# Performance work log

Hardware: AMD Instinct MI355X
Metric: run time of the kernel (lower is better)

The kernel has to match this reference:

```python
import jax, jax.numpy as jnp
from jax import lax
import numpy as np

RADIUS = 0.2
NSAMPLE = 32


def setup_inputs() -> dict:
    key = jax.random.key(0)
    ks = jax.random.split(key, 6)
    B, N, C = 4, 16384, 64
    xyz = jax.random.uniform(ks[0], (B, N, 3), dtype=jnp.float32)
    points = jax.random.normal(ks[1], (B, N, C), dtype=jnp.float32)
    w1 = jax.random.normal(ks[2], (64, C + 3), dtype=jnp.float32) * 0.05
    b1 = jnp.zeros((64,), jnp.float32)
    w2 = jax.random.normal(ks[3], (128, 64), dtype=jnp.float32) * 0.05
    b2 = jnp.zeros((128,), jnp.float32)
    return {"xyz": xyz, "points": points, "w1": w1, "b1": b1, "w2": w2, "b2": b2, "npoint": 1024}


def farthest_point_sampling(xyz, npoint):
    # xyz: (B,N,3). Deterministic start at index 0 (original uses a random start).
    B, N, _ = xyz.shape
    bidx = jnp.arange(B)

    def step(carry, _):
        distance, farthest = carry
        centroid = xyz[bidx, farthest]  # (B,3)
        dist = jnp.sum((xyz - centroid[:, None, :]) ** 2, axis=-1)  # (B,N)
        distance = jnp.minimum(distance, dist)
        nxt = jnp.argmax(distance, axis=-1)
        return (distance, nxt), farthest

    init = (jnp.full((B, N), 1e10, xyz.dtype), jnp.zeros((B,), jnp.int32))
    _, cents = lax.scan(step, init, None, length=npoint)  # (npoint,B)
    return cents.T  # (B,npoint)


def ball_query(xyz, new_xyz, radius, nsample):
    # xyz:(B,N,3) new_xyz:(B,S,3) -> (B,S,nsample) int indices
    N = xyz.shape[1]
    sqrdists = jnp.sum((new_xyz[:, :, None, :] - xyz[:, None, :, :]) ** 2, axis=-1)  # (B,S,N)
    idx = jnp.where(sqrdists > radius ** 2, N, jnp.arange(N))
    idx = jnp.sort(idx, axis=-1)[:, :, :nsample]
    first = idx[:, :, :1]
    return jnp.where(idx == N, first, idx)


def index_points(points, idx):
    # points:(B,N,C) idx:(B,...) -> (B,...,C)
    return jax.vmap(lambda p, i: p[i])(points, idx)


def reference(xyz, points, w1, b1, w2, b2, npoint):
    centroids = farthest_point_sampling(xyz, npoint)  # (B,S)
    new_xyz = index_points(xyz, centroids)  # (B,S,3)
    group_idx = ball_query(xyz, new_xyz, RADIUS, NSAMPLE)  # (B,S,K)
    grouped_xyz = index_points(xyz, group_idx)  # (B,S,K,3)
    grouped_xyz_norm = grouped_xyz - new_xyz[:, :, None, :]
    grouped_points = index_points(points, group_idx)  # (B,S,K,C)
    feats = jnp.concatenate([grouped_xyz_norm, grouped_points], axis=-1)  # (B,S,K,C+3)
    h = jax.nn.relu(jnp.einsum('bskc,oc->bsko', feats, w1) + b1)
    h = jax.nn.relu(jnp.einsum('bskc,oc->bsko', h, w2) + b2)  # (B,S,K,out)
    new_points = jnp.max(h, axis=2)  # (B,S,out)
    return (new_xyz, new_points)
```

## Files before the change

### kernel.cpp

```cpp
#include <hip/hip_runtime.h>

#define BB 4
#define NN 16384
#define CC 64
#define NPOINT 1024
#define NSAMPLE 32

#define FPS_T 1024
#define NCHUNK 256
#define NCELL 4096

#define REPEAT16(M) M(0) M(1) M(2) M(3) M(4) M(5) M(6) M(7) \
                    M(8) M(9) M(10) M(11) M(12) M(13) M(14) M(15)

__global__ __launch_bounds__(FPS_T) void fps_kernel(const float* __restrict__ xyz,
                                                    float* __restrict__ new_xyz,
                                                    float4* __restrict__ sorted) {
    #pragma clang fp contract(off)
    extern __shared__ char smem_raw[];
    float2* sxy  = (float2*)smem_raw;
    int*    hist = (int*)(smem_raw + 131072);
    float*  outc = (float*)(smem_raw + 131072);
    float*  lox  = (float*)(smem_raw + 147456);
    float*  loy  = lox + 272;
    float*  loz  = loy + 272;
    float*  hix  = loz + 272;
    float*  hiy  = hix + 272;
    float*  hiz  = hiy + 272;
    float4* wbc  = (float4*)(smem_raw + 153984);
    unsigned long long* slot = (unsigned long long*)(smem_raw + 154496);
    int*    wsum = (int*)(smem_raw + 154528);

    const int b    = blockIdx.x;
    const int tid  = threadIdx.x;
    const int lane = tid & 63;
    const int wv   = tid >> 6;
    const float* bx = xyz + (size_t)b * NN * 3;
    float4* sb = sorted + (size_t)b * NN;

    #pragma unroll
    for (int j = 0; j < 4; ++j) hist[j * FPS_T + tid] = 0;
    __syncthreads();

    #pragma unroll
    for (int j = 0; j < 16; ++j) {
        const int p = j * FPS_T + tid;
        const float x = bx[p * 3 + 0], y = bx[p * 3 + 1], z = bx[p * 3 + 2];
        int cx = (int)(x * 16.0f); cx = cx > 15 ? 15 : (cx < 0 ? 0 : cx);
        int cy = (int)(y * 16.0f); cy = cy > 15 ? 15 : (cy < 0 ? 0 : cy);
        int cz = (int)(z * 16.0f); cz = cz > 15 ? 15 : (cz < 0 ? 0 : cz);
        int code = 0;
        #pragma unroll
        for (int i = 0; i < 4; ++i)
            code |= (((cx >> i) & 1) << (3 * i)) |
                    (((cy >> i) & 1) << (3 * i + 1)) |
                    (((cz >> i) & 1) << (3 * i + 2));
        atomicAdd(&hist[code], 1);
    }
    __syncthreads();

    {
        const int h0 = hist[4 * tid + 0], h1 = hist[4 * tid + 1];
        const int h2 = hist[4 * tid + 2], h3 = hist[4 * tid + 3];
        const int s  = h0 + h1 + h2 + h3;
        int v = s;
        #pragma unroll
        for (int o = 1; o < 64; o <<= 1) {
            const int u = __shfl_up(v, o, 64);
            if (lane >= o) v += u;
        }
        if (lane == 63) wsum[wv] = v;
        __syncthreads();
        int base = 0;
        for (int w = 0; w < wv; ++w) base += wsum[w];
        const int e0 = base + v - s;
        hist[4 * tid + 0] = e0;
        hist[4 * tid + 1] = e0 + h0;
        hist[4 * tid + 2] = e0 + h0 + h1;
        hist[4 * tid + 3] = e0 + h0 + h1 + h2;
    }
    __syncthreads();

    #pragma unroll
    for (int j = 0; j < 16; ++j) {
        const int p = j * FPS_T + tid;
        const float x = bx[p * 3 + 0], y = bx[p * 3 + 1], z = bx[p * 3 + 2];
        int cx = (int)(x * 16.0f); cx = cx > 15 ? 15 : (cx < 0 ? 0 : cx);
        int cy = (int)(y * 16.0f); cy = cy > 15 ? 15 : (cy < 0 ? 0 : cy);
        int cz = (int)(z * 16.0f); cz = cz > 15 ? 15 : (cz < 0 ? 0 : cz);
        int code = 0;
        #pragma unroll
        for (int i = 0; i < 4; ++i)
            code |= (((cx >> i) & 1) << (3 * i)) |
                    (((cy >> i) & 1) << (3 * i + 1)) |
                    (((cz >> i) & 1) << (3 * i + 2));
        const int slotg = atomicAdd(&hist[code], 1);
        sb[slotg]  = make_float4(x, y, z, __int_as_float(p));
        sxy[slotg] = make_float2(x, y);
    }
    __syncthreads();

#define DECLZ(k) float z##k; unsigned long long key##k;
    REPEAT16(DECLZ)
#undef DECLZ
    float abx0 = 0.f, aby0 = 0.f, abz0 = 0.f, abx1 = 0.f, aby1 = 0.f, abz1 = 0.f;

#define AABBPRE(k) { const int g = wv + ((k) << 4);                       \
    const float4 pt = sb[(g << 6) + lane];                                \
    z##k = pt.z;                                                          \
    key##k = (((unsigned long long)__float_as_uint(1e10f)) << 32) |       \
             ((unsigned long long)(0x3FFFu -                              \
                    (unsigned)__float_as_int(pt.w)) << 4);                \
    float mnx = pt.x, mxx = pt.x, mny = pt.y, mxy = pt.y,                 \
          mnz = pt.z, mxz = pt.z;                                         \
    _Pragma("unroll")                                                     \
    for (int m = 32; m >= 1; m >>= 1) {                                   \
        mnx = fminf(mnx, __shfl_xor(mnx, m, 64));                         \
        mxx = fmaxf(mxx, __shfl_xor(mxx, m, 64));                         \
        mny = fminf(mny, __shfl_xor(mny, m, 64));                         \
        mxy = fmaxf(mxy, __shfl_xor(mxy, m, 64));                         \
        mnz = fminf(mnz, __shfl_xor(mnz, m, 64));                         \
        mxz = fmaxf(mxz, __shfl_xor(mxz, m, 64));                         \
    }                                                                     \
    if (lane == (k)) { abx0 = mnx; abx1 = mxx; aby0 = mny; aby1 = mxy;    \
                       abz0 = mnz; abz1 = mxz; } }
    REPEAT16(AABBPRE)
#undef AABBPRE
    if (tid == 0) { slot[0] = 0ull; slot[1] = 0ull; slot[2] = 0ull; slot[3] = 0ull; }
    __syncthreads();

    unsigned long long bkey = 0ull;
    int bestk = 0;
    int holder_ln = 0;
    float hx = 0.f, hy = 0.f, hz = 0.f;
    float cub = 1e10f;

    float ccx = bx[0], ccy = bx[1], ccz = bx[2];
    float prev_wd = 1e10f;

    for (int it = 0; it < NPOINT; ++it) {
        asm volatile("" : "+v"(z0), "+v"(z1), "+v"(z2),  "+v"(z3),
                          "+v"(z4), "+v"(z5), "+v"(z6),  "+v"(z7),
                          "+v"(z8), "+v"(z9), "+v"(z10), "+v"(z11),
                          "+v"(z12), "+v"(z13), "+v"(z14), "+v"(z15));

        if (tid == 0) {
            outc[it * 3 + 0] = ccx;
            outc[it * 3 + 1] = ccy;
            outc[it * 3 + 2] = ccz;
        }

        bool active = false;
        if (lane < 16) {
            const float dxl = fmaxf(fmaxf(abx0 - ccx, ccx - abx1), 0.0f);
            const float dyl = fmaxf(fmaxf(aby0 - ccy, ccy - aby1), 0.0f);
            const float dzl = fmaxf(fmaxf(abz0 - ccz, ccz - abz1), 0.0f);
            const float mind2 = dxl * dxl + dyl * dyl + dzl * dzl;
            const float bound = fminf(prev_wd, cub);
            active = !(mind2 > bound * 1.001f);
            if (active) {
                const float dxm = fmaxf(ccx - abx0, abx1 - ccx);
                const float dym = fmaxf(ccy - aby0, aby1 - ccy);
                const float dzm = fmaxf(ccz - abz0, abz1 - ccz);
                const float maxd2 = dxm * dxm + dym * dym + dzm * dzm;
                cub = fminf(cub, maxd2);
            }
        }
        const unsigned amask = (unsigned)(__ballot(active) & 0xFFFFull);

        bool lredo = false;
#define UPD(k) if (amask & (1u << (k))) {                                 \
            const int g = wv + ((k) << 4);                                \
            const float2 xy = sxy[(g << 6) + lane];                       \
            const float dx = xy.x - ccx;                                  \
            const float dy = xy.y - ccy;                                  \
            const float dz = z##k - ccz;                                  \
            const float t  = (dx * dx + dy * dy) + dz * dz;               \
            const float dold = __uint_as_float((unsigned)(key##k >> 32)); \
            if (t < dold) {                                               \
                key##k = (((unsigned long long)__float_as_uint(t)) << 32) \
                         | (key##k & 0xFFFFFFFFull);                      \
                lredo |= ((k) == bestk);                                  \
            }                                                             \
        }
        if (amask & 0x000Fu) { UPD(0)  UPD(1)  UPD(2)  UPD(3)  }
        if (amask & 0x00F0u) { UPD(4)  UPD(5)  UPD(6)  UPD(7)  }
        if (amask & 0x0F00u) { UPD(8)  UPD(9)  UPD(10) UPD(11) }
        if (amask & 0xF000u) { UPD(12) UPD(13) UPD(14) UPD(15) }
#undef UPD

        if (lredo) {
            bkey = 0ull; bestk = 0;
#define LM(k) if (key##k > bkey) { bkey = key##k; bestk = (k); }
            REPEAT16(LM)
#undef LM
        }

        const unsigned long long rb = __ballot(lredo);
        if ((rb >> holder_ln) & 1ull) {
            unsigned long long m = bkey;
            #pragma unroll
            for (int s = 32; s >= 1; s >>= 1) {
                const unsigned long long o = __shfl_xor(m, s, 64);
                m = o > m ? o : m;
            }
            holder_ln = __ffsll((long long)__ballot(bkey == m)) - 1;
            if (lane == holder_ln) {
                const float2 xy = sxy[((wv + (bestk << 4)) << 6) + lane];
                float zz = z0;
#define ZS(k) zz = (bestk == (k)) ? z##k : zz;
                REPEAT16(ZS)
#undef ZS
                hx = xy.x; hy = xy.y; hz = zz;
            }
        }

        if (lane == holder_ln) {
            wbc[(it & 1) * 16 + wv] = make_float4(hx, hy, hz, 0.0f);
            atomicMax(&slot[it & 3], bkey | (unsigned long long)wv);
        }
        if (tid == 0) slot[(it + 1) & 3] = 0ull;
        __syncthreads();

        const unsigned long long wk = slot[it & 3];
        prev_wd = __uint_as_float((unsigned)(wk >> 32));
        const int wwv = (int)(wk & 0xFull);
        const float4 wf = wbc[(it & 1) * 16 + wwv];
        ccx = wf.x; ccy = wf.y; ccz = wf.z;
    }

    __syncthreads();
    float* outb = new_xyz + (size_t)b * NPOINT * 3;
    #pragma unroll
    for (int j = 0; j < 3; ++j) {
        const int idx = j * FPS_T + tid;
        outb[idx] = outc[idx];
    }
}

__global__ __launch_bounds__(256) void ballq_kernel(const float* __restrict__ xyz,
                                                    const float* __restrict__ new_xyz,
                                                    int* __restrict__ gidx) {
    #pragma clang fp contract(off)
    const int lane = threadIdx.x & 63;
    const int q    = blockIdx.x * 4 + (threadIdx.x >> 6);
    const int b    = q >> 10;
    const float* bx = xyz + (size_t)b * NN * 3;
    const float* nx = new_xyz + (size_t)q * 3;
    const float cx = nx[0], cy = nx[1], cz = nx[2];
    const float rad2 = 0.04f;

    int* out  = gidx + (size_t)q * NSAMPLE;
    int taken = 0;
    int first = NN - 1;

    for (int chunk = 0; chunk < NN / 64 && taken < NSAMPLE; ++chunk) {
        const int   i  = chunk * 64 + lane;
        const float dx = cx - bx[i * 3 + 0];
        const float dy = cy - bx[i * 3 + 1];
        const float dz = cz - bx[i * 3 + 2];
        const float t  = dx * dx + dy * dy + dz * dz;
        const bool ok  = !(t > rad2);
        const unsigned long long m = __ballot(ok);
        const int cnt = __popcll(m);
        if (taken == 0 && cnt > 0) first = chunk * 64 + (__ffsll((long long)m) - 1);
        if (ok) {
            const int rank = taken + __popcll(m & ((1ull << lane) - 1ull));
            if (rank < NSAMPLE) out[rank] = i;
        }
        taken += cnt;
    }
    const int sat = taken < NSAMPLE ? taken : NSAMPLE;
    if (lane >= sat && lane < NSAMPLE) out[lane] = (taken > 0) ? first : (NN - 1);
}

__global__ __launch_bounds__(256) void mlp_kernel(const float* __restrict__ xyz,
                                                  const float* __restrict__ points,
                                                  const float* __restrict__ w1,
                                                  const float* __restrict__ b1,
                                                  const float* __restrict__ w2,
                                                  const float* __restrict__ b2,
                                                  const float* __restrict__ new_xyz,
                                                  const int*   __restrict__ gidx,
                                                  float* __restrict__ new_points) {
    __shared__ __align__(16) float feats[32][68];
    __shared__ __align__(16) float h1s[32][64];
    __shared__ float pmax[2][128];

    const int q = blockIdx.x;
    const int b = q >> 10;
    const int t = threadIdx.x;

    {
        const int k  = t >> 3;
        const int l8 = t & 7;
        const int gi = gidx[q * 32 + k];
        const float* prow = points + ((size_t)b * NN + gi) * CC;
        const float4 v0 = *(const float4*)(prow + l8 * 8);
        const float4 v1 = *(const float4*)(prow + l8 * 8 + 4);
        *(float4*)&feats[k][4 + l8 * 8] = v0;
        *(float4*)&feats[k][8 + l8 * 8] = v1;
        if (l8 == 0) {
            const float* pr = xyz + ((size_t)b * NN + gi) * 3;
            const float* nr = new_xyz + (size_t)q * 3;
            feats[k][0] = pr[0] - nr[0];
            feats[k][1] = pr[1] - nr[1];
            feats[k][2] = pr[2] - nr[2];
        }
    }

    const int c1 = t & 63;
    float w1r[67];
    #pragma unroll
    for (int j = 0; j < 67; ++j) w1r[j] = w1[c1 * 67 + j];
    const float bb1 = b1[c1];
    __syncthreads();

    const int kg = t >> 6;
    #pragma unroll
    for (int kk = 0; kk < 8; ++kk) {
        const int kr = kg * 8 + kk;
        float acc = bb1;
        acc += feats[kr][0] * w1r[0] + feats[kr][1] * w1r[1] + feats[kr][2] * w1r[2];
        #pragma unroll
        for (int j = 0; j < 64; j += 4) {
            const float4 f = *(const float4*)&feats[kr][4 + j];
            acc += f.x * w1r[3 + j] + f.y * w1r[4 + j] + f.z * w1r[5 + j] + f.w * w1r[6 + j];
        }
        h1s[kr][c1] = fmaxf(acc, 0.0f);
    }

    const int o2 = t & 127;
    const int kh = t >> 7;
    float w2r[64];
    #pragma unroll
    for (int j = 0; j < 64; ++j) w2r[j] = w2[o2 * 64 + j];
    const float bb2 = b2[o2];
    __syncthreads();

    float mx = -INFINITY;
    #pragma unroll
    for (int kk = 0; kk < 16; ++kk) {
        const int kr = kh * 16 + kk;
        float acc = bb2;
        #pragma unroll
        for (int j = 0; j < 64; j += 4) {
            const float4 h = *(const float4*)&h1s[kr][j];
            acc += h.x * w2r[j] + h.y * w2r[j + 1] + h.z * w2r[j + 2] + h.w * w2r[j + 3];
        }
        mx = fmaxf(mx, fmaxf(acc, 0.0f));
    }
    pmax[kh][o2] = mx;
    __syncthreads();
    if (t < 128) {
        new_points[(size_t)q * 128 + t] = fmaxf(pmax[0][t], pmax[1][t]);
    }
}

extern "C" void kernel_launch(void* const* d_in, const int* in_sizes, int n_in,
                              void* d_out, int out_size, void* d_ws, size_t ws_size,
                              hipStream_t stream) {
    const float* xyz    = (const float*)d_in[0];
    const float* points = (const float*)d_in[1];
    const float* w1     = (const float*)d_in[2];
    const float* b1     = (const float*)d_in[3];
    const float* w2     = (const float*)d_in[4];
    const float* b2     = (const float*)d_in[5];

    float* out_newxyz    = (float*)d_out;
    float* out_newpoints = (float*)d_out + (size_t)BB * NPOINT * 3;
    int*    gidx    = (int*)d_ws;
    float4* sortbuf = (float4*)((char*)d_ws + (size_t)512 * 1024);

    const int fps_lds = 154816;
    (void)hipFuncSetAttribute((const void*)fps_kernel,
                              hipFuncAttributeMaxDynamicSharedMemorySize,
                              fps_lds);

    fps_kernel<<<BB, FPS_T, fps_lds, stream>>>(xyz, out_newxyz, sortbuf);
    ballq_kernel<<<(BB * NPOINT) / 4, 256, 0, stream>>>(xyz, out_newxyz, gidx);
    mlp_kernel<<<BB * NPOINT, 256, 0, stream>>>(xyz, points, w1, b1, w2, b2,
                                                out_newxyz, gidx, out_newpoints);
}
```

Baseline: 1.590 ms.

## Halve FPS block to 8 waves with 32 chunks per lane and split argmax slots

The farthest-point-sampling kernel now runs with 512 threads (8 waves), so each lane holds 32 point chunks in registers instead of 16, with AABB culling extended to 32 chunks. The per-iteration cross-wave argmax uses four separate atomic slots, reduced after the barrier, and the winning centroid is broadcast by shuffling a speculatively loaded per-wave candidate. The aim is cheaper per-iteration barriers and less atomic contention in the serial 1024-step loop. In exchange each wave does twice the per-lane work and needs many more registers, which could cause spills.

```diff
diff --git a/kernel.cpp b/kernel.cpp
--- a/kernel.cpp
+++ b/kernel.cpp
@@ -6,30 +6,27 @@
 #define NPOINT 1024
 #define NSAMPLE 32
 
-#define FPS_T 1024
+#define FPS_T 512
+#define NWAVE 8
 #define NCHUNK 256
 #define NCELL 4096
 
-#define REPEAT16(M) M(0) M(1) M(2) M(3) M(4) M(5) M(6) M(7) \
-                    M(8) M(9) M(10) M(11) M(12) M(13) M(14) M(15)
-
-__global__ __launch_bounds__(FPS_T) void fps_kernel(const float* __restrict__ xyz,
-                                                    float* __restrict__ new_xyz,
-                                                    float4* __restrict__ sorted) {
+#define REPEAT32(M) M(0) M(1) M(2) M(3) M(4) M(5) M(6) M(7) \
+                    M(8) M(9) M(10) M(11) M(12) M(13) M(14) M(15) \
+                    M(16) M(17) M(18) M(19) M(20) M(21) M(22) M(23) \
+                    M(24) M(25) M(26) M(27) M(28) M(29) M(30) M(31)
+
+__global__ __launch_bounds__(FPS_T, 2) void fps_kernel(const float* __restrict__ xyz,
+                                                       float* __restrict__ new_xyz,
+                                                       float4* __restrict__ sorted) {
     #pragma clang fp contract(off)
     extern __shared__ char smem_raw[];
     float2* sxy  = (float2*)smem_raw;
     int*    hist = (int*)(smem_raw + 131072);
     float*  outc = (float*)(smem_raw + 131072);
-    float*  lox  = (float*)(smem_raw + 147456);
-    float*  loy  = lox + 272;
-    float*  loz  = loy + 272;
-    float*  hix  = loz + 272;
-    float*  hiy  = hix + 272;
-    float*  hiz  = hiy + 272;
-    float4* wbc  = (float4*)(smem_raw + 153984);
-    unsigned long long* slot = (unsigned long long*)(smem_raw + 154496);
-    int*    wsum = (int*)(smem_raw + 154528);
+    float4* wbc  = (float4*)(smem_raw + 147456);
+    unsigned long long* slot4 = (unsigned long long*)(smem_raw + 147712);
+    int*    wsum = (int*)(smem_raw + 147840);
 
     const int b    = blockIdx.x;
     const int tid  = threadIdx.x;
@@ -39,11 +36,11 @@
     float4* sb = sorted + (size_t)b * NN;
 
     #pragma unroll
-    for (int j = 0; j < 4; ++j) hist[j * FPS_T + tid] = 0;
-    __syncthreads();
-
-    #pragma unroll
-    for (int j = 0; j < 16; ++j) {
+    for (int j = 0; j < 8; ++j) hist[j * FPS_T + tid] = 0;
+    __syncthreads();
+
+    #pragma unroll
+    for (int j = 0; j < 32; ++j) {
         const int p = j * FPS_T + tid;
         const float x = bx[p * 3 + 0], y = bx[p * 3 + 1], z = bx[p * 3 + 2];
         int cx = (int)(x * 16.0f); cx = cx > 15 ? 15 : (cx < 0 ? 0 : cx);
@@ -60,9 +57,10 @@
     __syncthreads();
 
     {
-        const int h0 = hist[4 * tid + 0], h1 = hist[4 * tid + 1];
-        const int h2 = hist[4 * tid + 2], h3 = hist[4 * tid + 3];
-        const int s  = h0 + h1 + h2 + h3;
+        const int b8 = 8 * tid;
+        const int h0 = hist[b8+0], h1 = hist[b8+1], h2 = hist[b8+2], h3 = hist[b8+3];
+        const int h4 = hist[b8+4], h5 = hist[b8+5], h6 = hist[b8+6], h7 = hist[b8+7];
+        const int s  = h0 + h1 + h2 + h3 + h4 + h5 + h6 + h7;
         int v = s;
         #pragma unroll
         for (int o = 1; o < 64; o <<= 1) {
@@ -73,16 +71,20 @@
         __syncthreads();
         int base = 0;
         for (int w = 0; w < wv; ++w) base += wsum[w];
-        const int e0 = base + v - s;
-        hist[4 * tid + 0] = e0;
-        hist[4 * tid + 1] = e0 + h0;
-        hist[4 * tid + 2] = e0 + h0 + h1;
-        hist[4 * tid + 3] = e0 + h0 + h1 + h2;
-    }
-    __syncthreads();
-
-    #pragma unroll
-    for (int j = 0; j < 16; ++j) {
+        int e = base + v - s;
+        hist[b8+0] = e; e += h0;
+        hist[b8+1] = e; e += h1;
+        hist[b8+2] = e; e += h2;
+        hist[b8+3] = e; e += h3;
+        hist[b8+4] = e; e += h4;
+        hist[b8+5] = e; e += h5;
+        hist[b8+6] = e; e += h6;
+        hist[b8+7] = e;
+    }
+    __syncthreads();
+
+    #pragma unroll
+    for (int j = 0; j < 32; ++j) {
         const int p = j * FPS_T + tid;
         const float x = bx[p * 3 + 0], y = bx[p * 3 + 1], z = bx[p * 3 + 2];
         int cx = (int)(x * 16.0f); cx = cx > 15 ? 15 : (cx < 0 ? 0 : cx);
@@ -101,11 +103,11 @@
     __syncthreads();
 
 #define DECLZ(k) float z##k; unsigned long long key##k;
-    REPEAT16(DECLZ)
+    REPEAT32(DECLZ)
 #undef DECLZ
     float abx0 = 0.f, aby0 = 0.f, abz0 = 0.f, abx1 = 0.f, aby1 = 0.f, abz1 = 0.f;
 
-#define AABBPRE(k) { const int g = wv + ((k) << 4);                       \
+#define AABBPRE(k) { const int g = wv + ((k) << 3);                       \
     const float4 pt = sb[(g << 6) + lane];                                \
     z##k = pt.z;                                                          \
     key##k = (((unsigned long long)__float_as_uint(1e10f)) << 32) |       \
@@ -124,10 +126,19 @@
     }                                                                     \
     if (lane == (k)) { abx0 = mnx; abx1 = mxx; aby0 = mny; aby1 = mxy;    \
                        abz0 = mnz; abz1 = mxz; } }
-    REPEAT16(AABBPRE)
+    REPEAT32(AABBPRE)
 #undef AABBPRE
-    if (tid == 0) { slot[0] = 0ull; slot[1] = 0ull; slot[2] = 0ull; slot[3] = 0ull; }
-    __syncthreads();
+    if (tid < 16) slot4[tid] = 0ull;
+    __syncthreads();
+
+    asm volatile("" : "+v"(z0), "+v"(z1), "+v"(z2),  "+v"(z3),
+                      "+v"(z4), "+v"(z5), "+v"(z6),  "+v"(z7),
+                      "+v"(z8), "+v"(z9), "+v"(z10), "+v"(z11),
+                      "+v"(z12), "+v"(z13), "+v"(z14), "+v"(z15));
+    asm volatile("" : "+v"(z16), "+v"(z17), "+v"(z18), "+v"(z19),
+                      "+v"(z20), "+v"(z21), "+v"(z22), "+v"(z23),
+                      "+v"(z24), "+v"(z25), "+v"(z26), "+v"(z27),
+                      "+v"(z28), "+v"(z29), "+v"(z30), "+v"(z31));
 
     unsigned long long bkey = 0ull;
     int bestk = 0;
@@ -139,11 +150,6 @@
     float prev_wd = 1e10f;
 
     for (int it = 0; it < NPOINT; ++it) {
-        asm volatile("" : "+v"(z0), "+v"(z1), "+v"(z2),  "+v"(z3),
-                          "+v"(z4), "+v"(z5), "+v"(z6),  "+v"(z7),
-                          "+v"(z8), "+v"(z9), "+v"(z10), "+v"(z11),
-                          "+v"(z12), "+v"(z13), "+v"(z14), "+v"(z15));
-
         if (tid == 0) {
             outc[it * 3 + 0] = ccx;
             outc[it * 3 + 1] = ccy;
@@ -151,7 +157,7 @@
         }
 
         bool active = false;
-        if (lane < 16) {
+        if (lane < 32) {
             const float dxl = fmaxf(fmaxf(abx0 - ccx, ccx - abx1), 0.0f);
             const float dyl = fmaxf(fmaxf(aby0 - ccy, ccy - aby1), 0.0f);
             const float dzl = fmaxf(fmaxf(abz0 - ccz, ccz - abz1), 0.0f);
@@ -166,11 +172,11 @@
                 cub = fminf(cub, maxd2);
             }
         }
-        const unsigned amask = (unsigned)(__ballot(active) & 0xFFFFull);
+        const unsigned amask = (unsigned)(__ballot(active) & 0xFFFFFFFFull);
 
         bool lredo = false;
 #define UPD(k) if (amask & (1u << (k))) {                                 \
-            const int g = wv + ((k) << 4);                                \
+            const int g = wv + ((k) << 3);                                \
             const float2 xy = sxy[(g << 6) + lane];                       \
             const float dx = xy.x - ccx;                                  \
             const float dy = xy.y - ccy;                                  \
@@ -183,16 +189,20 @@
                 lredo |= ((k) == bestk);                                  \
             }                                                             \
         }
-        if (amask & 0x000Fu) { UPD(0)  UPD(1)  UPD(2)  UPD(3)  }
-        if (amask & 0x00F0u) { UPD(4)  UPD(5)  UPD(6)  UPD(7)  }
-        if (amask & 0x0F00u) { UPD(8)  UPD(9)  UPD(10) UPD(11) }
-        if (amask & 0xF000u) { UPD(12) UPD(13) UPD(14) UPD(15) }
+        if (amask & 0x0000000Fu) { UPD(0)  UPD(1)  UPD(2)  UPD(3)  }
+        if (amask & 0x000000F0u) { UPD(4)  UPD(5)  UPD(6)  UPD(7)  }
+        if (amask & 0x00000F00u) { UPD(8)  UPD(9)  UPD(10) UPD(11) }
+        if (amask & 0x0000F000u) { UPD(12) UPD(13) UPD(14) UPD(15) }
+        if (amask & 0x000F0000u) { UPD(16) UPD(17) UPD(18) UPD(19) }
+        if (amask & 0x00F00000u) { UPD(20) UPD(21) UPD(22) UPD(23) }
+        if (amask & 0x0F000000u) { UPD(24) UPD(25) UPD(26) UPD(27) }
+        if (amask & 0xF0000000u) { UPD(28) UPD(29) UPD(30) UPD(31) }
 #undef UPD
 
         if (lredo) {
             bkey = 0ull; bestk = 0;
 #define LM(k) if (key##k > bkey) { bkey = key##k; bestk = (k); }
-            REPEAT16(LM)
+            REPEAT32(LM)
 #undef LM
         }
 
@@ -206,33 +216,43 @@
             }
             holder_ln = __ffsll((long long)__ballot(bkey == m)) - 1;
             if (lane == holder_ln) {
-                const float2 xy = sxy[((wv + (bestk << 4)) << 6) + lane];
+                const float2 xy = sxy[((wv + (bestk << 3)) << 6) + lane];
                 float zz = z0;
 #define ZS(k) zz = (bestk == (k)) ? z##k : zz;
-                REPEAT16(ZS)
+                REPEAT32(ZS)
 #undef ZS
                 hx = xy.x; hy = xy.y; hz = zz;
             }
         }
 
         if (lane == holder_ln) {
-            wbc[(it & 1) * 16 + wv] = make_float4(hx, hy, hz, 0.0f);
-            atomicMax(&slot[it & 3], bkey | (unsigned long long)wv);
-        }
-        if (tid == 0) slot[(it + 1) & 3] = 0ull;
+            wbc[(it & 1) * 8 + wv] = make_float4(hx, hy, hz, 0.0f);
+            atomicMax(&slot4[(it & 3) * 4 + (wv & 3)],
+                      bkey | (unsigned long long)wv);
+        }
+        if (tid < 4) slot4[((it + 1) & 3) * 4 + tid] = 0ull;
         __syncthreads();
 
-        const unsigned long long wk = slot[it & 3];
+        const float4 spec = wbc[(it & 1) * 8 + (lane & 7)];
+        const unsigned long long s0 = slot4[(it & 3) * 4 + 0];
+        const unsigned long long s1 = slot4[(it & 3) * 4 + 1];
+        const unsigned long long s2 = slot4[(it & 3) * 4 + 2];
+        const unsigned long long s3 = slot4[(it & 3) * 4 + 3];
+        unsigned long long wk = s0;
+        if (s1 > wk) wk = s1;
+        if (s2 > wk) wk = s2;
+        if (s3 > wk) wk = s3;
         prev_wd = __uint_as_float((unsigned)(wk >> 32));
-        const int wwv = (int)(wk & 0xFull);
-        const float4 wf = wbc[(it & 1) * 16 + wwv];
-        ccx = wf.x; ccy = wf.y; ccz = wf.z;
+        const int wwv = (int)(wk & 0x7ull);
+        ccx = __shfl(spec.x, wwv, 64);
+        ccy = __shfl(spec.y, wwv, 64);
+        ccz = __shfl(spec.z, wwv, 64);
     }
 
     __syncthreads();
     float* outb = new_xyz + (size_t)b * NPOINT * 3;
     #pragma unroll
-    for (int j = 0; j < 3; ++j) {
+    for (int j = 0; j < 6; ++j) {
         const int idx = j * FPS_T + tid;
         outb[idx] = outc[idx];
     }
@@ -372,7 +392,7 @@
     int*    gidx    = (int*)d_ws;
     float4* sortbuf = (float4*)((char*)d_ws + (size_t)512 * 1024);
 
-    const int fps_lds = 154816;
+    const int fps_lds = 147904;
     (void)hipFuncSetAttribute((const void*)fps_kernel,
                               hipFuncAttributeMaxDynamicSharedMemorySize,
                               fps_lds);
```

Measured after the change: 2.181 ms. +37.1%, slower.

## Fuse FPS, ball query and MLP into one persistent kernel with progress flags

Applied to the files above, without the earlier changes.

Merges the three launches into one cooperative persistent kernel. Four blocks run farthest point sampling and publish each centroid plus a per-batch progress counter. The other 196 blocks poll that counter and run ball query and the MLP on groups of 8 centroids as soon as they exist, so the consumer work overlaps the serial FPS loop. Ball query now does a per-warp linear scan with early exit instead of the separate kernel. This risks spin-wait overhead, lower occupancy from 1024-thread blocks with large LDS, and deadlock if the blocks are not all co-resident in the fallback launch.

```diff
diff --git a/kernel.cpp b/kernel.cpp
--- a/kernel.cpp
+++ b/kernel.cpp
@@ -9,351 +9,359 @@
 #define FPS_T 1024
 #define NCHUNK 256
 #define NCELL 4096
+#define GRID_TOTAL 200
 
 #define REPEAT16(M) M(0) M(1) M(2) M(3) M(4) M(5) M(6) M(7) \
                     M(8) M(9) M(10) M(11) M(12) M(13) M(14) M(15)
 
-__global__ __launch_bounds__(FPS_T) void fps_kernel(const float* __restrict__ xyz,
-                                                    float* __restrict__ new_xyz,
-                                                    float4* __restrict__ sorted) {
-    #pragma clang fp contract(off)
+__global__ __launch_bounds__(FPS_T, 4) void fused_kernel(
+        const float* __restrict__ xyz, const float* __restrict__ points,
+        const float* __restrict__ w1,  const float* __restrict__ b1,
+        const float* __restrict__ w2,  const float* __restrict__ b2,
+        float* __restrict__ new_xyz,   float* __restrict__ new_points,
+        float4* __restrict__ sorted,   unsigned* __restrict__ prog) {
     extern __shared__ char smem_raw[];
-    float2* sxy  = (float2*)smem_raw;
-    int*    hist = (int*)(smem_raw + 131072);
-    float*  outc = (float*)(smem_raw + 131072);
-    float*  lox  = (float*)(smem_raw + 147456);
-    float*  loy  = lox + 272;
-    float*  loz  = loy + 272;
-    float*  hix  = loz + 272;
-    float*  hiy  = hix + 272;
-    float*  hiz  = hiy + 272;
-    float4* wbc  = (float4*)(smem_raw + 153984);
-    unsigned long long* slot = (unsigned long long*)(smem_raw + 154496);
-    int*    wsum = (int*)(smem_raw + 154528);
-
-    const int b    = blockIdx.x;
+
+    if (blockIdx.x < 4) {
+        #pragma clang fp contract(off)
+        float2* sxy  = (float2*)smem_raw;
+        int*    hist = (int*)(smem_raw + 131072);
+        float4* wbc  = (float4*)(smem_raw + 147456);
+        unsigned long long* slot = (unsigned long long*)(smem_raw + 147968);
+        int*    wsum = (int*)(smem_raw + 148000);
+
+        const int b    = blockIdx.x;
+        const int tid  = threadIdx.x;
+        const int lane = tid & 63;
+        const int wv   = tid >> 6;
+        const float* bx = xyz + (size_t)b * NN * 3;
+        float4* sb = sorted + (size_t)b * NN;
+        float* outg = new_xyz + (size_t)b * NPOINT * 3;
+
+        #pragma unroll
+        for (int j = 0; j < 4; ++j) hist[j * FPS_T + tid] = 0;
+        __syncthreads();
+
+        #pragma unroll
+        for (int j = 0; j < 16; ++j) {
+            const int p = j * FPS_T + tid;
+            const float x = bx[p * 3 + 0], y = bx[p * 3 + 1], z = bx[p * 3 + 2];
+            int cx = (int)(x * 16.0f); cx = cx > 15 ? 15 : (cx < 0 ? 0 : cx);
+            int cy = (int)(y * 16.0f); cy = cy > 15 ? 15 : (cy < 0 ? 0 : cy);
+            int cz = (int)(z * 16.0f); cz = cz > 15 ? 15 : (cz < 0 ? 0 : cz);
+            int code = 0;
+            #pragma unroll
+            for (int i = 0; i < 4; ++i)
+                code |= (((cx >> i) & 1) << (3 * i)) |
+                        (((cy >> i) & 1) << (3 * i + 1)) |
+                        (((cz >> i) & 1) << (3 * i + 2));
+            atomicAdd(&hist[code], 1);
+        }
+        __syncthreads();
+
+        {
+            const int h0 = hist[4 * tid + 0], h1 = hist[4 * tid + 1];
+            const int h2 = hist[4 * tid + 2], h3 = hist[4 * tid + 3];
+            const int s  = h0 + h1 + h2 + h3;
+            int v = s;
+            #pragma unroll
+            for (int o = 1; o < 64; o <<= 1) {
+                const int u = __shfl_up(v, o, 64);
+                if (lane >= o) v += u;
+            }
+            if (lane == 63) wsum[wv] = v;
+            __syncthreads();
+            int base = 0;
+            for (int w = 0; w < wv; ++w) base += wsum[w];
+            const int e0 = base + v - s;
+            hist[4 * tid + 0] = e0;
+            hist[4 * tid + 1] = e0 + h0;
+            hist[4 * tid + 2] = e0 + h0 + h1;
+            hist[4 * tid + 3] = e0 + h0 + h1 + h2;
+        }
+        __syncthreads();
+
+        #pragma unroll
+        for (int j = 0; j < 16; ++j) {
+            const int p = j * FPS_T + tid;
+            const float x = bx[p * 3 + 0], y = bx[p * 3 + 1], z = bx[p * 3 + 2];
+            int cx = (int)(x * 16.0f); cx = cx > 15 ? 15 : (cx < 0 ? 0 : cx);
+            int cy = (int)(y * 16.0f); cy = cy > 15 ? 15 : (cy < 0 ? 0 : cy);
+            int cz = (int)(z * 16.0f); cz = cz > 15 ? 15 : (cz < 0 ? 0 : cz);
+            int code = 0;
+            #pragma unroll
+            for (int i = 0; i < 4; ++i)
+                code |= (((cx >> i) & 1) << (3 * i)) |
+                        (((cy >> i) & 1) << (3 * i + 1)) |
+                        (((cz >> i) & 1) << (3 * i + 2));
+            const int slotg = atomicAdd(&hist[code], 1);
+            sb[slotg]  = make_float4(x, y, z, __int_as_float(p));
+            sxy[slotg] = make_float2(x, y);
+        }
+        __syncthreads();
+
+#define DECLZ(k) float z##k; unsigned long long key##k;
+        REPEAT16(DECLZ)
+#undef DECLZ
+        float abx0 = 0.f, aby0 = 0.f, abz0 = 0.f, abx1 = 0.f, aby1 = 0.f, abz1 = 0.f;
+
+#define AABBPRE(k) { const int g = wv + ((k) << 4);                       \
+        const float4 pt = sb[(g << 6) + lane];                            \
+        z##k = pt.z;                                                      \
+        key##k = (((unsigned long long)__float_as_uint(1e10f)) << 32) |   \
+                 ((unsigned long long)(0x3FFFu -                          \
+                        (unsigned)__float_as_int(pt.w)) << 4);            \
+        float mnx = pt.x, mxx = pt.x, mny = pt.y, mxy = pt.y,             \
+              mnz = pt.z, mxz = pt.z;                                     \
+        _Pragma("unroll")                                                 \
+        for (int m = 32; m >= 1; m >>= 1) {                               \
+            mnx = fminf(mnx, __shfl_xor(mnx, m, 64));                     \
+            mxx = fmaxf(mxx, __shfl_xor(mxx, m, 64));                     \
+            mny = fminf(mny, __shfl_xor(mny, m, 64));                     \
+            mxy = fmaxf(mxy, __shfl_xor(mxy, m, 64));                     \
+            mnz = fminf(mnz, __shfl_xor(mnz, m, 64));                     \
+            mxz = fmaxf(mxz, __shfl_xor(mxz, m, 64));                     \
+        }                                                                 \
+        if (lane == (k)) { abx0 = mnx; abx1 = mxx; aby0 = mny;            \
+                           aby1 = mxy; abz0 = mnz; abz1 = mxz; } }
+        REPEAT16(AABBPRE)
+#undef AABBPRE
+        if (tid < 4) slot[tid] = 0ull;
+        __syncthreads();
+
+        unsigned long long bkey = 0ull;
+        int bestk = 0;
+        int holder_ln = 0;
+        float hx = 0.f, hy = 0.f, hz = 0.f;
+        float cub = 1e10f;
+
+        float ccx = bx[0], ccy = bx[1], ccz = bx[2];
+        float prev_wd = 1e10f;
+
+        for (int it = 0; it < NPOINT; ++it) {
+            asm volatile("" : "+v"(z0), "+v"(z1), "+v"(z2),  "+v"(z3),
+                              "+v"(z4), "+v"(z5), "+v"(z6),  "+v"(z7),
+                              "+v"(z8), "+v"(z9), "+v"(z10), "+v"(z11),
+                              "+v"(z12), "+v"(z13), "+v"(z14), "+v"(z15));
+
+            if (wv == (it & 15) && lane == 0) {
+                unsigned* og = (unsigned*)(outg + it * 3);
+                __hip_atomic_store(og + 0, __float_as_uint(ccx),
+                                   __ATOMIC_RELAXED, __HIP_MEMORY_SCOPE_AGENT);
+                __hip_atomic_store(og + 1, __float_as_uint(ccy),
+                                   __ATOMIC_RELAXED, __HIP_MEMORY_SCOPE_AGENT);
+                __hip_atomic_store(og + 2, __float_as_uint(ccz),
+                                   __ATOMIC_RELAXED, __HIP_MEMORY_SCOPE_AGENT);
+                __hip_atomic_store(&prog[b], (unsigned)(it + 1),
+                                   __ATOMIC_RELEASE, __HIP_MEMORY_SCOPE_AGENT);
+            }
+
+            bool active = false;
+            if (lane < 16) {
+                const float dxl = fmaxf(fmaxf(abx0 - ccx, ccx - abx1), 0.0f);
+                const float dyl = fmaxf(fmaxf(aby0 - ccy, ccy - aby1), 0.0f);
+                const float dzl = fmaxf(fmaxf(abz0 - ccz, ccz - abz1), 0.0f);
+                const float mind2 = dxl * dxl + dyl * dyl + dzl * dzl;
+                const float bound = fminf(prev_wd, cub);
+                active = !(mind2 > bound * 1.001f);
+                if (active) {
+                    const float dxm = fmaxf(ccx - abx0, abx1 - ccx);
+                    const float dym = fmaxf(ccy - aby0, aby1 - ccy);
+                    const float dzm = fmaxf(ccz - abz0, abz1 - ccz);
+                    const float maxd2 = dxm * dxm + dym * dym + dzm * dzm;
+                    cub = fminf(cub, maxd2);
+                }
+            }
+            const unsigned amask = (unsigned)(__ballot(active) & 0xFFFFull);
+
+            bool lredo = false;
+#define UPD(k) if (amask & (1u << (k))) {                                 \
+                const int g = wv + ((k) << 4);                            \
+                const float2 xy = sxy[(g << 6) + lane];                   \
+                const float dx = xy.x - ccx;                              \
+                const float dy = xy.y - ccy;                              \
+                const float dz = z##k - ccz;                              \
+                const float t  = (dx * dx + dy * dy) + dz * dz;           \
+                const float dold = __uint_as_float((unsigned)(key##k >> 32)); \
+                if (t < dold) {                                           \
+                    key##k = (((unsigned long long)__float_as_uint(t)) << 32) \
+                             | (key##k & 0xFFFFFFFFull);                  \
+                    lredo |= ((k) == bestk);                              \
+                }                                                         \
+            }
+            if (amask & 0x000Fu) { UPD(0)  UPD(1)  UPD(2)  UPD(3)  }
+            if (amask & 0x00F0u) { UPD(4)  UPD(5)  UPD(6)  UPD(7)  }
+            if (amask & 0x0F00u) { UPD(8)  UPD(9)  UPD(10) UPD(11) }
+            if (amask & 0xF000u) { UPD(12) UPD(13) UPD(14) UPD(15) }
+#undef UPD
+
+            if (lredo) {
+                bkey = 0ull; bestk = 0;
+#define LM(k) if (key##k > bkey) { bkey = key##k; bestk = (k); }
+                REPEAT16(LM)
+#undef LM
+            }
+
+            const unsigned long long rb = __ballot(lredo);
+            if ((rb >> holder_ln) & 1ull) {
+                unsigned long long m = bkey;
+                #pragma unroll
+                for (int s = 32; s >= 1; s >>= 1) {
+                    const unsigned long long o = __shfl_xor(m, s, 64);
+                    m = o > m ? o : m;
+                }
+                holder_ln = __ffsll((long long)__ballot(bkey == m)) - 1;
+                if (lane == holder_ln) {
+                    const float2 xy = sxy[((wv + (bestk << 4)) << 6) + lane];
+                    float zz = z0;
+#define ZS(k) zz = (bestk == (k)) ? z##k : zz;
+                    REPEAT16(ZS)
+#undef ZS
+                    hx = xy.x; hy = xy.y; hz = zz;
+                }
+            }
+
+            if (lane == holder_ln) {
+                wbc[(it & 1) * 16 + wv] = make_float4(hx, hy, hz, 0.0f);
+                atomicMax(&slot[it & 3], bkey | (unsigned long long)wv);
+            }
+            if (tid == 0) slot[(it + 1) & 3] = 0ull;
+            __syncthreads();
+
+            const unsigned long long wk = slot[it & 3];
+            prev_wd = __uint_as_float((unsigned)(wk >> 32));
+            const int wwv = (int)(wk & 0xFull);
+            const float4 wf = wbc[(it & 1) * 16 + wwv];
+            ccx = wf.x; ccy = wf.y; ccz = wf.z;
+        }
+        return;
+    }
+
+    float* feats = (float*)smem_raw;
+    float* h1s   = (float*)(smem_raw + 69632);
+    int*   sgidx = (int*)(smem_raw + 135168);
+
+    const int ci   = blockIdx.x - 4;
+    const int NC   = (int)gridDim.x - 4;
     const int tid  = threadIdx.x;
     const int lane = tid & 63;
-    const int wv   = tid >> 6;
-    const float* bx = xyz + (size_t)b * NN * 3;
-    float4* sb = sorted + (size_t)b * NN;
-
-    #pragma unroll
-    for (int j = 0; j < 4; ++j) hist[j * FPS_T + tid] = 0;
-    __syncthreads();
-
-    #pragma unroll
-    for (int j = 0; j < 16; ++j) {
-        const int p = j * FPS_T + tid;
-        const float x = bx[p * 3 + 0], y = bx[p * 3 + 1], z = bx[p * 3 + 2];
-        int cx = (int)(x * 16.0f); cx = cx > 15 ? 15 : (cx < 0 ? 0 : cx);
-        int cy = (int)(y * 16.0f); cy = cy > 15 ? 15 : (cy < 0 ? 0 : cy);
-        int cz = (int)(z * 16.0f); cz = cz > 15 ? 15 : (cz < 0 ? 0 : cz);
-        int code = 0;
-        #pragma unroll
-        for (int i = 0; i < 4; ++i)
-            code |= (((cx >> i) & 1) << (3 * i)) |
-                    (((cy >> i) & 1) << (3 * i + 1)) |
-                    (((cz >> i) & 1) << (3 * i + 2));
-        atomicAdd(&hist[code], 1);
-    }
-    __syncthreads();
-
-    {
-        const int h0 = hist[4 * tid + 0], h1 = hist[4 * tid + 1];
-        const int h2 = hist[4 * tid + 2], h3 = hist[4 * tid + 3];
-        const int s  = h0 + h1 + h2 + h3;
-        int v = s;
-        #pragma unroll
-        for (int o = 1; o < 64; o <<= 1) {
-            const int u = __shfl_up(v, o, 64);
-            if (lane >= o) v += u;
-        }
-        if (lane == 63) wsum[wv] = v;
-        __syncthreads();
-        int base = 0;
-        for (int w = 0; w < wv; ++w) base += wsum[w];
-        const int e0 = base + v - s;
-        hist[4 * tid + 0] = e0;
-        hist[4 * tid + 1] = e0 + h0;
-        hist[4 * tid + 2] = e0 + h0 + h1;
-        hist[4 * tid + 3] = e0 + h0 + h1 + h2;
-    }
-    __syncthreads();
-
-    #pragma unroll
-    for (int j = 0; j < 16; ++j) {
-        const int p = j * FPS_T + tid;
-        const float x = bx[p * 3 + 0], y = bx[p * 3 + 1], z = bx[p * 3 + 2];
-        int cx = (int)(x * 16.0f); cx = cx > 15 ? 15 : (cx < 0 ? 0 : cx);
-        int cy = (int)(y * 16.0f); cy = cy > 15 ? 15 : (cy < 0 ? 0 : cy);
-        int cz = (int)(z * 16.0f); cz = cz > 15 ? 15 : (cz < 0 ? 0 : cz);
-        int code = 0;
-        #pragma unroll
-        for (int i = 0; i < 4; ++i)
-            code |= (((cx >> i) & 1) << (3 * i)) |
-                    (((cy >> i) & 1) << (3 * i + 1)) |
-                    (((cz >> i) & 1) << (3 * i + 2));
-        const int slotg = atomicAdd(&hist[code], 1);
-        sb[slotg]  = make_float4(x, y, z, __int_as_float(p));
-        sxy[slotg] = make_float2(x, y);
-    }
-    __syncthreads();
-
-#define DECLZ(k) float z##k; unsigned long long key##k;
-    REPEAT16(DECLZ)
-#undef DECLZ
-    float abx0 = 0.f, aby0 = 0.f, abz0 = 0.f, abx1 = 0.f, aby1 = 0.f, abz1 = 0.f;
-
-#define AABBPRE(k) { const int g = wv + ((k) << 4);                       \
-    const float4 pt = sb[(g << 6) + lane];                                \
-    z##k = pt.z;                                                          \
-    key##k = (((unsigned long long)__float_as_uint(1e10f)) << 32) |       \
-             ((unsigned long long)(0x3FFFu -                              \
-                    (unsigned)__float_as_int(pt.w)) << 4);                \
-    float mnx = pt.x, mxx = pt.x, mny = pt.y, mxy = pt.y,                 \
-          mnz = pt.z, mxz = pt.z;                                         \
-    _Pragma("unroll")                                                     \
-    for (int m = 32; m >= 1; m >>= 1) {                                   \
-        mnx = fminf(mnx, __shfl_xor(mnx, m, 64));                         \
-        mxx = fmaxf(mxx, __shfl_xor(mxx, m, 64));                         \
-        mny = fminf(mny, __shfl_xor(mny, m, 64));                         \
-        mxy = fmaxf(mxy, __shfl_xor(mxy, m, 64));                         \
-        mnz = fminf(mnz, __shfl_xor(mnz, m, 64));                         \
-        mxz = fmaxf(mxz, __shfl_xor(mxz, m, 64));                         \
-    }                                                                     \
-    if (lane == (k)) { abx0 = mnx; abx1 = mxx; aby0 = mny; aby1 = mxy;    \
-                       abz0 = mnz; abz1 = mxz; } }
-    REPEAT16(AABBPRE)
-#undef AABBPRE
-    if (tid == 0) { slot[0] = 0ull; slot[1] = 0ull; slot[2] = 0ull; slot[3] = 0ull; }
-    __syncthreads();
-
-    unsigned long long bkey = 0ull;
-    int bestk = 0;
-    int holder_ln = 0;
-    float hx = 0.f, hy = 0.f, hz = 0.f;
-    float cub = 1e10f;
-
-    float ccx = bx[0], ccy = bx[1], ccz = bx[2];
-    float prev_wd = 1e10f;
-
-    for (int it = 0; it < NPOINT; ++it) {
-        asm volatile("" : "+v"(z0), "+v"(z1), "+v"(z2),  "+v"(z3),
-                          "+v"(z4), "+v"(z5), "+v"(z6),  "+v"(z7),
-                          "+v"(z8), "+v"(z9), "+v"(z10), "+v"(z11),
-                          "+v"(z12), "+v"(z13), "+v"(z14), "+v"(z15));
+    const int pr   = tid >> 7;
+    const int pl   = tid & 127;
+    const int wi   = (tid >> 6) & 1;
+
+    for (int q0 = ci * 8; q0 < BB * NPOINT; q0 += NC * 8) {
+        const int b     = q0 >> 10;
+        const int maxiq = (q0 + 7) & 1023;
 
         if (tid == 0) {
-            outc[it * 3 + 0] = ccx;
-            outc[it * 3 + 1] = ccy;
-            outc[it * 3 + 2] = ccz;
-        }
-
-        bool active = false;
-        if (lane < 16) {
-            const float dxl = fmaxf(fmaxf(abx0 - ccx, ccx - abx1), 0.0f);
-            const float dyl = fmaxf(fmaxf(aby0 - ccy, ccy - aby1), 0.0f);
-            const float dzl = fmaxf(fmaxf(abz0 - ccz, ccz - abz1), 0.0f);
-            const float mind2 = dxl * dxl + dyl * dyl + dzl * dzl;
-            const float bound = fminf(prev_wd, cub);
-            active = !(mind2 > bound * 1.001f);
-            if (active) {
-                const float dxm = fmaxf(ccx - abx0, abx1 - ccx);
-                const float dym = fmaxf(ccy - aby0, aby1 - ccy);
-                const float dzm = fmaxf(ccz - abz0, abz1 - ccz);
-                const float maxd2 = dxm * dxm + dym * dym + dzm * dzm;
-                cub = fminf(cub, maxd2);
-            }
-        }
-        const unsigned amask = (unsigned)(__ballot(active) & 0xFFFFull);
-
-        bool lredo = false;
-#define UPD(k) if (amask & (1u << (k))) {                                 \
-            const int g = wv + ((k) << 4);                                \
-            const float2 xy = sxy[(g << 6) + lane];                       \
-            const float dx = xy.x - ccx;                                  \
-            const float dy = xy.y - ccy;                                  \
-            const float dz = z##k - ccz;                                  \
-            const float t  = (dx * dx + dy * dy) + dz * dz;               \
-            const float dold = __uint_as_float((unsigned)(key##k >> 32)); \
-            if (t < dold) {                                               \
-                key##k = (((unsigned long long)__float_as_uint(t)) << 32) \
-                         | (key##k & 0xFFFFFFFFull);                      \
-                lredo |= ((k) == bestk);                                  \
-            }                                                             \
-        }
-        if (amask & 0x000Fu) { UPD(0)  UPD(1)  UPD(2)  UPD(3)  }
-        if (amask & 0x00F0u) { UPD(4)  UPD(5)  UPD(6)  UPD(7)  }
-        if (amask & 0x0F00u) { UPD(8)  UPD(9)  UPD(10) UPD(11) }
-        if (amask & 0xF000u) { UPD(12) UPD(13) UPD(14) UPD(15) }
-#undef UPD
-
-        if (lredo) {
-            bkey = 0ull; bestk = 0;
-#define LM(k) if (key##k > bkey) { bkey = key##k; bestk = (k); }
-            REPEAT16(LM)
-#undef LM
-        }
-
-        const unsigned long long rb = __ballot(lredo);
-        if ((rb >> holder_ln) & 1ull) {
-            unsigned long long m = bkey;
-            #pragma unroll
-            for (int s = 32; s >= 1; s >>= 1) {
-                const unsigned long long o = __shfl_xor(m, s, 64);
-                m = o > m ? o : m;
-            }
-            holder_ln = __ffsll((long long)__ballot(bkey == m)) - 1;
-            if (lane == holder_ln) {
-                const float2 xy = sxy[((wv + (bestk << 4)) << 6) + lane];
-                float zz = z0;
-#define ZS(k) zz = (bestk == (k)) ? z##k : zz;
-                REPEAT16(ZS)
-#undef ZS
-                hx = xy.x; hy = xy.y; hz = zz;
-            }
-        }
-
-        if (lane == holder_ln) {
-            wbc[(it & 1) * 16 + wv] = make_float4(hx, hy, hz, 0.0f);
-            atomicMax(&slot[it & 3], bkey | (unsigned long long)wv);
-        }
-        if (tid == 0) slot[(it + 1) & 3] = 0ull;
-        __syncthreads();
-
-        const unsigned long long wk = slot[it & 3];
-        prev_wd = __uint_as_float((unsigned)(wk >> 32));
-        const int wwv = (int)(wk & 0xFull);
-        const float4 wf = wbc[(it & 1) * 16 + wwv];
-        ccx = wf.x; ccy = wf.y; ccz = wf.z;
-    }
-
-    __syncthreads();
-    float* outb = new_xyz + (size_t)b * NPOINT * 3;
-    #pragma unroll
-    for (int j = 0; j < 3; ++j) {
-        const int idx = j * FPS_T + tid;
-        outb[idx] = outc[idx];
-    }
-}
-
-__global__ __launch_bounds__(256) void ballq_kernel(const float* __restrict__ xyz,
-                                                    const float* __restrict__ new_xyz,
-                                                    int* __restrict__ gidx) {
-    #pragma clang fp contract(off)
-    const int lane = threadIdx.x & 63;
-    const int q    = blockIdx.x * 4 + (threadIdx.x >> 6);
-    const int b    = q >> 10;
-    const float* bx = xyz + (size_t)b * NN * 3;
-    const float* nx = new_xyz + (size_t)q * 3;
-    const float cx = nx[0], cy = nx[1], cz = nx[2];
-    const float rad2 = 0.04f;
-
-    int* out  = gidx + (size_t)q * NSAMPLE;
-    int taken = 0;
-    int first = NN - 1;
-
-    for (int chunk = 0; chunk < NN / 64 && taken < NSAMPLE; ++chunk) {
-        const int   i  = chunk * 64 + lane;
-        const float dx = cx - bx[i * 3 + 0];
-        const float dy = cy - bx[i * 3 + 1];
-        const float dz = cz - bx[i * 3 + 2];
-        const float t  = dx * dx + dy * dy + dz * dz;
-        const bool ok  = !(t > rad2);
-        const unsigned long long m = __ballot(ok);
-        const int cnt = __popcll(m);
-        if (taken == 0 && cnt > 0) first = chunk * 64 + (__ffsll((long long)m) - 1);
-        if (ok) {
-            const int rank = taken + __popcll(m & ((1ull << lane) - 1ull));
-            if (rank < NSAMPLE) out[rank] = i;
-        }
-        taken += cnt;
-    }
-    const int sat = taken < NSAMPLE ? taken : NSAMPLE;
-    if (lane >= sat && lane < NSAMPLE) out[lane] = (taken > 0) ? first : (NN - 1);
-}
-
-__global__ __launch_bounds__(256) void mlp_kernel(const float* __restrict__ xyz,
-                                                  const float* __restrict__ points,
-                                                  const float* __restrict__ w1,
-                                                  const float* __restrict__ b1,
-                                                  const float* __restrict__ w2,
-                                                  const float* __restrict__ b2,
-                                                  const float* __restrict__ new_xyz,
-                                                  const int*   __restrict__ gidx,
-                                                  float* __restrict__ new_points) {
-    __shared__ __align__(16) float feats[32][68];
-    __shared__ __align__(16) float h1s[32][64];
-    __shared__ float pmax[2][128];
-
-    const int q = blockIdx.x;
-    const int b = q >> 10;
-    const int t = threadIdx.x;
-
-    {
-        const int k  = t >> 3;
-        const int l8 = t & 7;
-        const int gi = gidx[q * 32 + k];
-        const float* prow = points + ((size_t)b * NN + gi) * CC;
-        const float4 v0 = *(const float4*)(prow + l8 * 8);
-        const float4 v1 = *(const float4*)(prow + l8 * 8 + 4);
-        *(float4*)&feats[k][4 + l8 * 8] = v0;
-        *(float4*)&feats[k][8 + l8 * 8] = v1;
-        if (l8 == 0) {
-            const float* pr = xyz + ((size_t)b * NN + gi) * 3;
-            const float* nr = new_xyz + (size_t)q * 3;
-            feats[k][0] = pr[0] - nr[0];
-            feats[k][1] = pr[1] - nr[1];
-            feats[k][2] = pr[2] - nr[2];
-        }
-    }
-
-    const int c1 = t & 63;
-    float w1r[67];
-    #pragma unroll
-    for (int j = 0; j < 67; ++j) w1r[j] = w1[c1 * 67 + j];
-    const float bb1 = b1[c1];
-    __syncthreads();
-
-    const int kg = t >> 6;
-    #pragma unroll
-    for (int kk = 0; kk < 8; ++kk) {
-        const int kr = kg * 8 + kk;
-        float acc = bb1;
-        acc += feats[kr][0] * w1r[0] + feats[kr][1] * w1r[1] + feats[kr][2] * w1r[2];
-        #pragma unroll
-        for (int j = 0; j < 64; j += 4) {
-            const float4 f = *(const float4*)&feats[kr][4 + j];
-            acc += f.x * w1r[3 + j] + f.y * w1r[4 + j] + f.z * w1r[5 + j] + f.w * w1r[6 + j];
-        }
-        h1s[kr][c1] = fmaxf(acc, 0.0f);
-    }
-
-    const int o2 = t & 127;
-    const int kh = t >> 7;
-    float w2r[64];
-    #pragma unroll
-    for (int j = 0; j < 64; ++j) w2r[j] = w2[o2 * 64 + j];
-    const float bb2 = b2[o2];
-    __syncthreads();
-
-    float mx = -INFINITY;
-    #pragma unroll
-    for (int kk = 0; kk < 16; ++kk) {
-        const int kr = kh * 16 + kk;
-        float acc = bb2;
-        #pragma unroll
-        for (int j = 0; j < 64; j += 4) {
-            const float4 h = *(const float4*)&h1s[kr][j];
-            acc += h.x * w2r[j] + h.y * w2r[j + 1] + h.z * w2r[j + 2] + h.w * w2r[j + 3];
-        }
-        mx = fmaxf(mx, fmaxf(acc, 0.0f));
-    }
-    pmax[kh][o2] = mx;
-    __syncthreads();
-    if (t < 128) {
-        new_points[(size_t)q * 128 + t] = fmaxf(pmax[0][t], pmax[1][t]);
+            while ((int)__hip_atomic_load(&prog[b], __ATOMIC_ACQUIRE,
+                                          __HIP_MEMORY_SCOPE_AGENT) <= maxiq)
+                __builtin_amdgcn_s_sleep(10);
+        }
+        __syncthreads();
+
+        const int q = q0 + pr;
+        const unsigned* cg = (const unsigned*)(new_xyz + (size_t)q * 3);
+        const float cx = __uint_as_float(__hip_atomic_load(cg + 0,
+                __ATOMIC_RELAXED, __HIP_MEMORY_SCOPE_AGENT));
+        const float cy = __uint_as_float(__hip_atomic_load(cg + 1,
+                __ATOMIC_RELAXED, __HIP_MEMORY_SCOPE_AGENT));
+        const float cz = __uint_as_float(__hip_atomic_load(cg + 2,
+                __ATOMIC_RELAXED, __HIP_MEMORY_SCOPE_AGENT));
+
+        if (wi == 0) {
+            #pragma clang fp contract(off)
+            const float* bx = xyz + (size_t)b * NN * 3;
+            const float rad2 = 0.04f;
+            int* out  = sgidx + pr * 32;
+            int taken = 0;
+            int first = NN - 1;
+            for (int chunk = 0; chunk < NN / 64 && taken < NSAMPLE; ++chunk) {
+                const int   i  = chunk * 64 + lane;
+                const float dx = cx - bx[i * 3 + 0];
+                const float dy = cy - bx[i * 3 + 1];
+                const float dz = cz - bx[i * 3 + 2];
+                const float t  = dx * dx + dy * dy + dz * dz;
+                const bool ok  = !(t > rad2);
+                const unsigned long long m = __ballot(ok);
+                const int cnt = __popcll(m);
+                if (taken == 0 && cnt > 0)
+                    first = chunk * 64 + (__ffsll((long long)m) - 1);
+                if (ok) {
+                    const int rank = taken + __popcll(m & ((1ull << lane) - 1ull));
+                    if (rank < NSAMPLE) out[rank] = i;
+                }
+                taken += cnt;
+            }
+            const int sat = taken < NSAMPLE ? taken : NSAMPLE;
+            if (lane >= sat && lane < NSAMPLE)
+                out[lane] = (taken > 0) ? first : (NN - 1);
+        }
+        __syncthreads();
+
+        {
+            const int k  = pl >> 2;
+            const int l4 = pl & 3;
+            const int gi = sgidx[pr * 32 + k];
+            const float* prow = points + ((size_t)b * NN + gi) * CC;
+            float* fr = feats + (size_t)(pr * 32 + k) * 68;
+            #pragma unroll
+            for (int u = 0; u < 4; ++u)
+                *(float4*)(fr + 4 + l4 * 16 + u * 4) =
+                    *(const float4*)(prow + l4 * 16 + u * 4);
+            if (l4 == 0) {
+                const float* pxyz = xyz + ((size_t)b * NN + gi) * 3;
+                fr[0] = pxyz[0] - cx;
+                fr[1] = pxyz[1] - cy;
+                fr[2] = pxyz[2] - cz;
+            }
+        }
+        __syncthreads();
+
+        {
+            const int c1 = lane;
+            float w1r[67];
+            #pragma unroll
+            for (int j = 0; j < 67; ++j) w1r[j] = w1[c1 * 67 + j];
+            const float bb1 = b1[c1];
+            #pragma unroll
+            for (int kk = 0; kk < 16; ++kk) {
+                const int kr = wi * 16 + kk;
+                const float* fr = feats + (size_t)(pr * 32 + kr) * 68;
+                float acc = bb1;
+                acc += fr[0] * w1r[0] + fr[1] * w1r[1] + fr[2] * w1r[2];
+                #pragma unroll
+                for (int j = 0; j < 64; j += 4) {
+                    const float4 f = *(const float4*)(fr + 4 + j);
+                    acc += f.x * w1r[3 + j] + f.y * w1r[4 + j]
+                         + f.z * w1r[5 + j] + f.w * w1r[6 + j];
+                }
+                h1s[(size_t)(pr * 32 + kr) * 64 + c1] = fmaxf(acc, 0.0f);
+            }
+        }
+        __syncthreads();
+
+        {
+            float w2r[64];
+            #pragma unroll
+            for (int j = 0; j < 64; ++j) w2r[j] = w2[pl * 64 + j];
+            const float bb2 = b2[pl];
+            float mx = -INFINITY;
+            #pragma unroll
+            for (int kr = 0; kr < 32; ++kr) {
+                const float* hr = h1s + (size_t)(pr * 32 + kr) * 64;
+                float acc = bb2;
+                #pragma unroll
+                for (int j = 0; j < 64; j += 4) {
+                    const float4 h = *(const float4*)(hr + j);
+                    acc += h.x * w2r[j] + h.y * w2r[j + 1]
+                         + h.z * w2r[j + 2] + h.w * w2r[j + 3];
+                }
+                mx = fmaxf(mx, fmaxf(acc, 0.0f));
+            }
+            new_points[(size_t)q * 128 + pl] = mx;
+        }
+        __syncthreads();
     }
 }
 
@@ -369,16 +377,25 @@
 
     float* out_newxyz    = (float*)d_out;
     float* out_newpoints = (float*)d_out + (size_t)BB * NPOINT * 3;
-    int*    gidx    = (int*)d_ws;
-    float4* sortbuf = (float4*)((char*)d_ws + (size_t)512 * 1024);
-
-    const int fps_lds = 154816;
-    (void)hipFuncSetAttribute((const void*)fps_kernel,
+    unsigned* prog   = (unsigned*)d_ws;
+    float4*   sortbuf = (float4*)((char*)d_ws + 1024);
+
+    (void)hipMemsetAsync(prog, 0, 4 * sizeof(unsigned), stream);
+
+    const unsigned fused_lds = 148160;
+    (void)hipFuncSetAttribute((const void*)fused_kernel,
                               hipFuncAttributeMaxDynamicSharedMemorySize,
-                              fps_lds);
-
-    fps_kernel<<<BB, FPS_T, fps_lds, stream>>>(xyz, out_newxyz, sortbuf);
-    ballq_kernel<<<(BB * NPOINT) / 4, 256, 0, stream>>>(xyz, out_newxyz, gidx);
-    mlp_kernel<<<BB * NPOINT, 256, 0, stream>>>(xyz, points, w1, b1, w2, b2,
-                                                out_newxyz, gidx, out_newpoints);
+                              (int)fused_lds);
+
+    void* args[] = {(void*)&xyz, (void*)&points, (void*)&w1, (void*)&b1,
+                    (void*)&w2, (void*)&b2, (void*)&out_newxyz,
+                    (void*)&out_newpoints, (void*)&sortbuf, (void*)&prog};
+    hipError_t err = hipLaunchCooperativeKernel(
+        (const void*)fused_kernel, dim3(GRID_TOTAL), dim3(FPS_T),
+        args, fused_lds, stream);
+    if (err != hipSuccess) {
+        fused_kernel<<<dim3(GRID_TOTAL), dim3(FPS_T), fused_lds, stream>>>(
+            xyz, points, w1, b1, w2, b2, out_newxyz, out_newpoints,
+            sortbuf, prog);
+    }
 }
```

Result: slower. 3.027 ms (+90.4%).
